# Kernel tuning notes

Measured on AMD Instinct MI355X. Metric: run time of the kernel, lower is better.

The kernel has to match this reference:

```python
import jax, jax.numpy as jnp
import numpy as np

N = 50000   # nodes
E = 800000  # edges
IN, HID, HEADS, OUT = 128, 32, 4, 64
NEG_SLOPE = 0.2


def _gatv2_layer(x, src, dst, Wl, bl, Wr, br, att, bias, res_W, concat):
    """One PyG-style GATv2Conv layer (eval mode, no dropout).
    x: [N, F_in]; att: [H, C]. Returns [N, H*C] if concat else [N, C]."""
    H, C = att.shape
    xl = (x @ Wl + bl).reshape(N, H, C)   # source transform
    xr = (x @ Wr + br).reshape(N, H, C)   # target transform
    e = jax.nn.leaky_relu(xl[src] + xr[dst], NEG_SLOPE)        # [E, H, C]
    logit = jnp.einsum('ehc,hc->eh', e, att)                   # [E, H]
    # segment softmax over incoming edges per destination node
    m = jax.ops.segment_max(logit, dst, num_segments=N)        # [N, H]
    p = jnp.exp(logit - m[dst])
    denom = jax.ops.segment_sum(p, dst, num_segments=N)
    alpha = p / (denom[dst] + 1e-16)                           # [E, H]
    out = jax.ops.segment_sum(xl[src] * alpha[:, :, None], dst, num_segments=N)  # [N, H, C]
    out = out.reshape(N, H * C) if concat else out.mean(axis=1)
    if res_W is not None:
        out = out + x @ res_W
    return out + bias


def _glorot(key, shape):
    fan_in = shape[0] if len(shape) > 1 else shape[-1]
    return jax.random.normal(key, shape, dtype=jnp.float32) / np.sqrt(fan_in)


def setup_inputs() -> dict:
    key = jax.random.key(0)
    ks = iter(jax.random.split(key, 32))
    x = jax.random.normal(next(ks), (N, IN), dtype=jnp.float32)
    edge_index = jax.random.randint(next(ks), (2, E), 0, N, dtype=jnp.int64)
    d = {"x": x, "edge_index": edge_index}
    HC = HEADS * HID  # 128
    # layer 0: IN -> HEADS*HID, concat, residual
    d["Wl0"] = _glorot(next(ks), (IN, HC)); d["bl0"] = jnp.zeros((HC,), jnp.float32)
    d["Wr0"] = _glorot(next(ks), (IN, HC)); d["br0"] = jnp.zeros((HC,), jnp.float32)
    d["att0"] = _glorot(next(ks), (HEADS, HID)); d["b0"] = jnp.zeros((HC,), jnp.float32)
    d["res0"] = _glorot(next(ks), (IN, HC))
    # layer 1: HC -> HEADS*HID, concat, residual
    d["Wl1"] = _glorot(next(ks), (HC, HC)); d["bl1"] = jnp.zeros((HC,), jnp.float32)
    d["Wr1"] = _glorot(next(ks), (HC, HC)); d["br1"] = jnp.zeros((HC,), jnp.float32)
    d["att1"] = _glorot(next(ks), (HEADS, HID)); d["b1"] = jnp.zeros((HC,), jnp.float32)
    d["res1"] = _glorot(next(ks), (HC, HC))
    # layer 2: HC -> OUT, heads=1, concat=False, no residual
    d["Wl2"] = _glorot(next(ks), (HC, OUT)); d["bl2"] = jnp.zeros((OUT,), jnp.float32)
    d["Wr2"] = _glorot(next(ks), (HC, OUT)); d["br2"] = jnp.zeros((OUT,), jnp.float32)
    d["att2"] = _glorot(next(ks), (1, OUT)); d["b2"] = jnp.zeros((OUT,), jnp.float32)
    return d


def reference(x, edge_index,
              Wl0, bl0, Wr0, br0, att0, b0, res0,
              Wl1, bl1, Wr1, br1, att1, b1, res1,
              Wl2, bl2, Wr2, br2, att2, b2):
    src, dst = edge_index[0], edge_index[1]
    h = _gatv2_layer(x, src, dst, Wl0, bl0, Wr0, br0, att0, b0, res0, True)
    h = jax.nn.elu(h)
    h = _gatv2_layer(h, src, dst, Wl1, bl1, Wr1, br1, att1, b1, res1, True)
    h = jax.nn.elu(h)
    return _gatv2_layer(h, src, dst, Wl2, bl2, Wr2, br2, att2, b2, None, False)
```

## Files before the change

### kernel.cpp

```cpp
#include <hip/hip_runtime.h>
#include <math.h>

#define NN 50000
#define EE 800000
#define NBK 196
#define EPB 4096

typedef short v8s __attribute__((ext_vector_type(8)));
typedef float v4f __attribute__((ext_vector_type(4)));

__device__ __forceinline__ ushort f2bf(float f) {
    uint u = __float_as_uint(f);
    uint r = (u + 0x7fffu + ((u >> 16) & 1u)) >> 16;
    return (ushort)r;
}
__device__ __forceinline__ float bf2f(ushort h) {
    return __uint_as_float(((uint)h) << 16);
}
__device__ __forceinline__ float lrelu(float x) {
    return fmaf(0.4f, fabsf(x), 0.6f * x);
}

__device__ __forceinline__ void gld_lds16(const void* g, void* l) {
    __builtin_amdgcn_global_load_lds(
        (const __attribute__((address_space(1))) void*)g,
        (__attribute__((address_space(3))) void*)l, 16, 0, 0);
}

template <int CTRL>
__device__ __forceinline__ float dppadd(float x) {
    int y = __builtin_amdgcn_update_dpp(0, __float_as_int(x), CTRL, 0xf, 0xf, true);
    return x + __int_as_float(y);
}
__device__ __forceinline__ float sum8(float x) {
    x = dppadd<0xB1>(x);
    x = dppadd<0x4E>(x);
    x = dppadd<0x141>(x);
    return x;
}
__device__ __forceinline__ float sum16(float x) {
    x = sum8(x);
    x = dppadd<0x140>(x);
    return x;
}
__device__ __forceinline__ float expclamp(float t) {
    return __expf(fminf(fmaxf(t, -60.f), 80.f));
}

__global__ __launch_bounds__(256) void k_bktcnt(const int* __restrict__ edst,
                                                int* __restrict__ bcnt) {
    __shared__ int h[NBK];
    int t = threadIdx.x;
    if (t < NBK) h[t] = 0;
    __syncthreads();
    int eb = blockIdx.x * EPB;
    #pragma unroll
    for (int k = 0; k < EPB / 256; ++k) {
        int e = eb + k * 256 + t;
        if (e < EE) atomicAdd(&h[edst[e] >> 8], 1);
    }
    __syncthreads();
    if (t < NBK && h[t]) atomicAdd(&bcnt[t], h[t]);
}

__global__ __launch_bounds__(256) void k_bscan(const int* __restrict__ bcnt,
                                               int* __restrict__ bbase,
                                               int* __restrict__ bcur) {
    __shared__ int sm[256];
    int t = threadIdx.x;
    int v = (t < NBK) ? bcnt[t] : 0;
    sm[t] = v;
    __syncthreads();
    for (int o = 1; o < 256; o <<= 1) {
        int a = (t >= o) ? sm[t - o] : 0;
        __syncthreads();
        sm[t] += a;
        __syncthreads();
    }
    if (t < NBK) { int ex = sm[t] - v; bbase[t] = ex; bcur[t] = ex; }
}

__global__ __launch_bounds__(256) void k_bktplace(const int* __restrict__ esrc,
                                                  const int* __restrict__ edst,
                                                  int* __restrict__ bcur,
                                                  uint* __restrict__ ebuf) {
    __shared__ int h[NBK];
    __shared__ int base[NBK];
    int t = threadIdx.x;
    if (t < NBK) h[t] = 0;
    __syncthreads();
    int eb = blockIdx.x * EPB;
    int pk[EPB / 256];
    #pragma unroll
    for (int k = 0; k < EPB / 256; ++k) {
        int e = eb + k * 256 + t;
        pk[k] = -1;
        if (e < EE) {
            int b = edst[e] >> 8;
            int r = atomicAdd(&h[b], 1);
            pk[k] = (b << 16) | r;
        }
    }
    __syncthreads();
    if (t < NBK && h[t]) base[t] = atomicAdd(&bcur[t], h[t]);
    __syncthreads();
    #pragma unroll
    for (int k = 0; k < EPB / 256; ++k) {
        int e = eb + k * 256 + t;
        if (e < EE) {
            int b = pk[k] >> 16;
            int r = pk[k] & 0xFFFF;
            uint dl = (uint)(edst[e] & 255);
            ebuf[base[b] + r] = (dl << 16) | (uint)esrc[e];
        }
    }
}

__global__ __launch_bounds__(256) void k_bktfin(const uint* __restrict__ ebuf,
                                                const int* __restrict__ bbase,
                                                const int* __restrict__ bcnt,
                                                int* __restrict__ rowptr,
                                                int* __restrict__ csrc) {
    __shared__ int deg[256];
    __shared__ int sm[256];
    __shared__ int cur[256];
    const int b = blockIdx.x;
    const int t = threadIdx.x;
    const int eb = bbase[b];
    const int ec = bcnt[b];
    deg[t] = 0;
    __syncthreads();
    for (int k = t; k < ec; k += 256)
        atomicAdd(&deg[ebuf[eb + k] >> 16], 1);
    __syncthreads();
    int v = deg[t];
    sm[t] = v;
    __syncthreads();
    for (int o = 1; o < 256; o <<= 1) {
        int a = (t >= o) ? sm[t - o] : 0;
        __syncthreads();
        sm[t] += a;
        __syncthreads();
    }
    int node = b * 256 + t;
    if (node < NN) rowptr[node + 1] = eb + sm[t];
    if (node == 0) rowptr[0] = 0;
    cur[t] = sm[t] - v;
    __syncthreads();
    for (int k = t; k < ec; k += 256) {
        uint u = ebuf[eb + k];
        int nl = (int)(u >> 16);
        int r = atomicAdd(&cur[nl], 1);
        csrc[eb + r] = (int)(u & 0xFFFFu);
    }
}

struct WPack {
    const float* W[8];
    ushort* Th[8];
    ushort* Tl[8];
    int fout[8];
};

__global__ __launch_bounds__(256) void k_conv_w(WPack p) {
    int wi = blockIdx.y;
    int fout = p.fout[wi];
    int total = 128 * fout;
    int i = blockIdx.x * 256 + threadIdx.x;
    if (i >= total) return;
    int k = i / fout;
    int n = i - k * fout;
    float f = p.W[wi][i];
    ushort h = f2bf(f);
    float lo = f - bf2f(h);
    int t = n >> 4, m = n & 15, c = k >> 5, quad = (k >> 3) & 3, j = k & 7;
    int flat = ((((t * 4 + c) * 4 + quad) * 16 + m) << 3) + j;
    p.Th[wi][flat] = h;
    p.Tl[wi][flat] = f2bf(lo);
}

template <int FOUT, int NMAT, bool CVT, int TS>
__global__ __launch_bounds__(512) void k_gemm_fused(
    const float* __restrict__ Xf,
    const ushort* __restrict__ Xh, const ushort* __restrict__ Xl,
    const ushort* __restrict__ T0h, const ushort* __restrict__ T0l, const float* __restrict__ B0,
    const ushort* __restrict__ T1h, const ushort* __restrict__ T1l, const float* __restrict__ B1,
    const ushort* __restrict__ T2h, const ushort* __restrict__ T2l,
    const float* __restrict__ ATT, float* __restrict__ DL, float* __restrict__ DR,
    ushort* __restrict__ O0b, float* __restrict__ O1, float* __restrict__ O2)
{
    constexpr int CH = TS * 2048;
    __shared__ __align__(16) ushort Bs[NMAT * 2 * CH];

    const int tid  = threadIdx.x;
    const int lane = tid & 63;
    const int wid  = tid >> 6;
    const int m    = lane & 15;
    const int quad = lane >> 4;
    const int row0 = blockIdx.x * 128 + wid * 16;
    const int t0   = blockIdx.y * TS;

    {
        const ushort* tbls[6] = {T0h, T0l, T1h, T1l, T2h, T2l};
        #pragma unroll
        for (int k = 0; k < 2 * NMAT; ++k) {
            gld_lds16(tbls[k] + (size_t)t0 * 2048 + (size_t)tid * 8,
                      &Bs[k * CH + tid * 8]);
        }
    }

    v8s ah[4], al[4];
    {
        int arow = row0 + m;
        if (arow > NN - 1) arow = NN - 1;
        #pragma unroll
        for (int c = 0; c < 4; ++c) {
            size_t off = (size_t)arow * 128 + c * 32 + quad * 8;
            if constexpr (CVT) {
                float4 f0 = *(const float4*)(Xf + off);
                float4 f1 = *(const float4*)(Xf + off + 4);
                const float fe[8] = {f0.x, f0.y, f0.z, f0.w, f1.x, f1.y, f1.z, f1.w};
                #pragma unroll
                for (int e = 0; e < 8; ++e) {
                    ushort h = f2bf(fe[e]);
                    float lo = fe[e] - bf2f(h);
                    ah[c][e] = (short)h;
                    al[c][e] = (short)(__float_as_uint(lo) >> 16);
                }
            } else {
                ah[c] = *(const v8s*)(Xh + off);
                al[c] = *(const v8s*)(Xl + off);
            }
        }
    }

    __syncthreads();

    float dp0[4] = {0.f, 0.f, 0.f, 0.f};
    float dp1[4] = {0.f, 0.f, 0.f, 0.f};

    #pragma unroll
    for (int tt = 0; tt < TS; ++tt) {
        const int t = t0 + tt;
        v4f a0 = {0.f, 0.f, 0.f, 0.f};
        v4f a1 = {0.f, 0.f, 0.f, 0.f};
        v4f a2 = {0.f, 0.f, 0.f, 0.f};
        #pragma unroll
        for (int c = 0; c < 4; ++c) {
            const int fo = tt * 2048 + (c * 4 + quad) * 128 + m * 8;
            v8s b0h = *(const v8s*)&Bs[0 * CH + fo];
            v8s b0l = *(const v8s*)&Bs[1 * CH + fo];
            v8s b1h = *(const v8s*)&Bs[2 * CH + fo];
            v8s b1l = *(const v8s*)&Bs[3 * CH + fo];
            a0 = __builtin_amdgcn_mfma_f32_16x16x32_bf16(al[c], b0h, a0, 0, 0, 0);
            a1 = __builtin_amdgcn_mfma_f32_16x16x32_bf16(al[c], b1h, a1, 0, 0, 0);
            a0 = __builtin_amdgcn_mfma_f32_16x16x32_bf16(ah[c], b0l, a0, 0, 0, 0);
            a1 = __builtin_amdgcn_mfma_f32_16x16x32_bf16(ah[c], b1l, a1, 0, 0, 0);
            a0 = __builtin_amdgcn_mfma_f32_16x16x32_bf16(ah[c], b0h, a0, 0, 0, 0);
            a1 = __builtin_amdgcn_mfma_f32_16x16x32_bf16(ah[c], b1h, a1, 0, 0, 0);
            if constexpr (NMAT == 3) {
                v8s b2h = *(const v8s*)&Bs[4 * CH + fo];
                v8s b2l = *(const v8s*)&Bs[5 * CH + fo];
                a2 = __builtin_amdgcn_mfma_f32_16x16x32_bf16(al[c], b2h, a2, 0, 0, 0);
                a2 = __builtin_amdgcn_mfma_f32_16x16x32_bf16(ah[c], b2l, a2, 0, 0, 0);
                a2 = __builtin_amdgcn_mfma_f32_16x16x32_bf16(ah[c], b2h, a2, 0, 0, 0);
            }
        }
        const int col = t * 16 + m;
        const float bad0 = B0[col];
        const float bad1 = B1[col];
        const float attc = ATT[col];
        #pragma unroll
        for (int j = 0; j < 4; ++j) {
            float o0v = a0[j] + bad0;
            float o1v = a1[j] + bad1;
            dp0[j] = fmaf(attc, o0v, dp0[j]);
            dp1[j] = fmaf(attc, o1v, dp1[j]);
            int r = row0 + quad * 4 + j;
            if (r < NN) {
                O0b[(size_t)r * FOUT + col] = f2bf(o0v);
                O1[(size_t)r * FOUT + col] = o1v;
                if constexpr (NMAT == 3) O2[(size_t)r * FOUT + col] = a2[j];
            }
        }
        if constexpr (FOUT == 128) {
            if ((t & 1) == 1) {
                const int h = t >> 1;
                #pragma unroll
                for (int j = 0; j < 4; ++j) {
                    float s0 = sum16(dp0[j]);
                    float s1 = sum16(dp1[j]);
                    int r = row0 + quad * 4 + j;
                    if (m == 0 && r < NN) {
                        DL[(size_t)r * 4 + h] = 0.6f * s0;
                        DR[(size_t)r * 4 + h] = 0.6f * s1;
                    }
                    dp0[j] = 0.f;
                    dp1[j] = 0.f;
                }
            }
        }
    }
    if constexpr (FOUT == 64) {
        #pragma unroll
        for (int j = 0; j < 4; ++j) {
            float s0 = sum16(dp0[j]);
            float s1 = sum16(dp1[j]);
            int r = row0 + quad * 4 + j;
            if (m == 0 && r < NN) {
                atomicAdd(&DL[r], 0.6f * s0);
                atomicAdd(&DR[r], 0.6f * s1);
            }
        }
    }
}

__global__ __launch_bounds__(256) void k_agg01(const ushort* __restrict__ XLb,
                                               const float4* __restrict__ XR4,
                                               const float4* __restrict__ RES4,
                                               const float* __restrict__ att,
                                               const float* __restrict__ bias,
                                               const float* __restrict__ DL,
                                               const float* __restrict__ DR,
                                               const int* __restrict__ rowptr,
                                               const int* __restrict__ csrc,
                                               ushort* __restrict__ Hh,
                                               ushort* __restrict__ Hl) {
    const int lane = threadIdx.x & 63;
    const int wid = threadIdx.x >> 6;
    const int n = blockIdx.x * 4 + wid;
    if (n >= NN) return;
    const int beg = rowptr[n];
    const int end = rowptr[n + 1];
    const int half = lane >> 5;
    const uint j = lane & 31;
    const uint head = j >> 3;

    const float4 xr = XR4[(uint)n * 32u + j];
    float4 at = ((const float4*)att)[j];
    at.x *= 0.4f; at.y *= 0.4f; at.z *= 0.4f; at.w *= 0.4f;
    const float dRn = DR[(uint)n * 4u + head];
    float4 s = {0.f, 0.f, 0.f, 0.f};
    float d = 0.f;

#define EDGE01(U, DLV)  {                                             \
    float4 v = {bf2f((U).x), bf2f((U).y), bf2f((U).z), bf2f((U).w)};  \
    float t0 =      at.x * fabsf(v.x + xr.x);                         \
    t0 = fmaf(at.y, fabsf(v.y + xr.y), t0);                           \
    t0 = fmaf(at.z, fabsf(v.z + xr.z), t0);                           \
    t0 = fmaf(at.w, fabsf(v.w + xr.w), t0);                           \
    float p = expclamp(sum8(t0) + (DLV) + dRn);                       \
    d += p;                                                            \
    s.x = fmaf(p, v.x, s.x); s.y = fmaf(p, v.y, s.y);                 \
    s.z = fmaf(p, v.z, s.z); s.w = fmaf(p, v.w, s.w); }

    int i = beg;
    for (; i + 8 <= end; i += 8) {
        uint sa = (uint)csrc[i + half];
        uint sb = (uint)csrc[i + 2 + half];
        uint sc = (uint)csrc[i + 4 + half];
        uint sd = (uint)csrc[i + 6 + half];
        ushort4 ua = *(const ushort4*)(XLb + (size_t)sa * 128u + 4u * j);
        float  da_ = DL[(size_t)sa * 4u + head];
        ushort4 ub = *(const ushort4*)(XLb + (size_t)sb * 128u + 4u * j);
        float  db_ = DL[(size_t)sb * 4u + head];
        ushort4 uc = *(const ushort4*)(XLb + (size_t)sc * 128u + 4u * j);
        float  dc_ = DL[(size_t)sc * 4u + head];
        ushort4 ud = *(const ushort4*)(XLb + (size_t)sd * 128u + 4u * j);
        float  dd_ = DL[(size_t)sd * 4u + head];
        EDGE01(ua, da_)
        EDGE01(ub, db_)
        EDGE01(uc, dc_)
        EDGE01(ud, dd_)
    }
    for (; i < end; i += 2) {
        int ia = i + half;
        if (ia > end - 1) ia = end - 1;
        uint sa = (uint)csrc[ia];
        ushort4 ua = *(const ushort4*)(XLb + (size_t)sa * 128u + 4u * j);
        float  da_ = DL[(size_t)sa * 4u + head];
        float4 v = {bf2f(ua.x), bf2f(ua.y), bf2f(ua.z), bf2f(ua.w)};
        float t0 =      at.x * fabsf(v.x + xr.x);
        t0 = fmaf(at.y, fabsf(v.y + xr.y), t0);
        t0 = fmaf(at.z, fabsf(v.z + xr.z), t0);
        t0 = fmaf(at.w, fabsf(v.w + xr.w), t0);
        float p = expclamp(sum8(t0) + da_ + dRn);
        if (half && (i + 1 >= end)) p = 0.f;
        d += p;
        s.x = fmaf(p, v.x, s.x); s.y = fmaf(p, v.y, s.y);
        s.z = fmaf(p, v.z, s.z); s.w = fmaf(p, v.w, s.w);
    }
#undef EDGE01

    d   += __shfl_xor(d, 32);
    s.x += __shfl_xor(s.x, 32);
    s.y += __shfl_xor(s.y, 32);
    s.z += __shfl_xor(s.z, 32);
    s.w += __shfl_xor(s.w, 32);

    if (half == 0) {
        float inv = (d > 0.f) ? 1.f / d : 0.f;
        float4 rv = RES4[(uint)n * 32u + j];
        float4 bv = ((const float4*)bias)[j];
        float o0 = fmaf(s.x, inv, rv.x + bv.x);
        float o1 = fmaf(s.y, inv, rv.y + bv.y);
        float o2 = fmaf(s.z, inv, rv.z + bv.z);
        float o3 = fmaf(s.w, inv, rv.w + bv.w);
        o0 = o0 > 0.f ? o0 : __expf(o0) - 1.f;
        o1 = o1 > 0.f ? o1 : __expf(o1) - 1.f;
        o2 = o2 > 0.f ? o2 : __expf(o2) - 1.f;
        o3 = o3 > 0.f ? o3 : __expf(o3) - 1.f;
        ushort4 h, l;
        h.x = f2bf(o0); l.x = f2bf(o0 - bf2f(h.x));
        h.y = f2bf(o1); l.y = f2bf(o1 - bf2f(h.y));
        h.z = f2bf(o2); l.z = f2bf(o2 - bf2f(h.z));
        h.w = f2bf(o3); l.w = f2bf(o3 - bf2f(h.w));
        *(ushort4*)(Hh + (uint)n * 128u + 4u * j) = h;
        *(ushort4*)(Hl + (uint)n * 128u + 4u * j) = l;
    }
}

__global__ __launch_bounds__(256) void k_agg2(const ushort* __restrict__ XLb,
                                              const float4* __restrict__ XR4,
                                              const float* __restrict__ att,
                                              const float* __restrict__ bias,
                                              const float* __restrict__ DL,
                                              const float* __restrict__ DR,
                                              const int* __restrict__ rowptr,
                                              const int* __restrict__ csrc,
                                              float* __restrict__ OUT) {
    const int lane = threadIdx.x & 63;
    const int wid = threadIdx.x >> 6;
    const int n = blockIdx.x * 4 + wid;
    if (n >= NN) return;
    const int beg = rowptr[n];
    const int end = rowptr[n + 1];
    const int q = lane >> 4;
    const uint jj = lane & 15;

    const float4 xr = XR4[(uint)n * 16u + jj];
    float4 at = ((const float4*)att)[jj];
    at.x *= 0.4f; at.y *= 0.4f; at.z *= 0.4f; at.w *= 0.4f;
    const float dRn = DR[n];
    float4 s = {0.f, 0.f, 0.f, 0.f};
    float d = 0.f;
    const int e1 = end - 1;

    for (int i = beg; i < end; i += 8) {
        int i0 = i + q;
        int i1 = i + 4 + q;
        uint s0 = (uint)csrc[min(i0, e1)];
        uint s1 = (uint)csrc[min(i1, e1)];
        ushort4 u0 = *(const ushort4*)(XLb + (size_t)s0 * 64u + 4u * jj);
        float  dl0 = DL[s0];
        ushort4 u1 = *(const ushort4*)(XLb + (size_t)s1 * 64u + 4u * jj);
        float  dl1 = DL[s1];
        #pragma unroll
        for (int u = 0; u < 2; ++u) {
            ushort4 uv = (u == 0) ? u0 : u1;
            float  dlv = (u == 0) ? dl0 : dl1;
            int ii = (u == 0) ? i0 : i1;
            float4 v = {bf2f(uv.x), bf2f(uv.y), bf2f(uv.z), bf2f(uv.w)};
            float t0 =      at.x * fabsf(v.x + xr.x);
            t0 = fmaf(at.y, fabsf(v.y + xr.y), t0);
            t0 = fmaf(at.z, fabsf(v.z + xr.z), t0);
            t0 = fmaf(at.w, fabsf(v.w + xr.w), t0);
            float p = expclamp(sum16(t0) + dlv + dRn);
            if (ii >= end) p = 0.f;
            d += p;
            s.x = fmaf(p, v.x, s.x); s.y = fmaf(p, v.y, s.y);
            s.z = fmaf(p, v.z, s.z); s.w = fmaf(p, v.w, s.w);
        }
    }

    d   += __shfl_xor(d, 16);   d   += __shfl_xor(d, 32);
    s.x += __shfl_xor(s.x, 16); s.x += __shfl_xor(s.x, 32);
    s.y += __shfl_xor(s.y, 16); s.y += __shfl_xor(s.y, 32);
    s.z += __shfl_xor(s.z, 16); s.z += __shfl_xor(s.z, 32);
    s.w += __shfl_xor(s.w, 16); s.w += __shfl_xor(s.w, 32);

    if (lane < 16) {
        float inv = (d > 0.f) ? 1.f / d : 0.f;
        float4 bv = ((const float4*)bias)[jj];
        float4 o;
        o.x = fmaf(s.x, inv, bv.x);
        o.y = fmaf(s.y, inv, bv.y);
        o.z = fmaf(s.z, inv, bv.z);
        o.w = fmaf(s.w, inv, bv.w);
        *(float4*)(OUT + (uint)n * 64u + 4u * jj) = o;
    }
}

extern "C" void kernel_launch(void* const* d_in, const int* in_sizes, int n_in,
                              void* d_out, int out_size, void* d_ws, size_t ws_size,
                              hipStream_t stream) {
    const float* x    = (const float*)d_in[0];
    const int*   ei   = (const int*)d_in[1];
    const int*   esrc = ei;
    const int*   edst = ei + EE;

    const float* Wl0 = (const float*)d_in[2];
    const float* bl0 = (const float*)d_in[3];
    const float* Wr0 = (const float*)d_in[4];
    const float* br0 = (const float*)d_in[5];
    const float* at0 = (const float*)d_in[6];
    const float* b0  = (const float*)d_in[7];
    const float* rs0 = (const float*)d_in[8];
    const float* Wl1 = (const float*)d_in[9];
    const float* bl1 = (const float*)d_in[10];
    const float* Wr1 = (const float*)d_in[11];
    const float* br1 = (const float*)d_in[12];
    const float* at1 = (const float*)d_in[13];
    const float* b1  = (const float*)d_in[14];
    const float* rs1 = (const float*)d_in[15];
    const float* Wl2 = (const float*)d_in[16];
    const float* bl2 = (const float*)d_in[17];
    const float* Wr2 = (const float*)d_in[18];
    const float* br2 = (const float*)d_in[19];
    const float* at2 = (const float*)d_in[20];
    const float* b2  = (const float*)d_in[21];

    float* out = (float*)d_out;

    ushort* XLb = (ushort*)d_ws;
    float* XR  = (float*)(XLb + (size_t)NN * 128);
    float* RES = XR + (size_t)NN * 128;
    ushort* Xh = (ushort*)(RES + (size_t)NN * 128);
    ushort* Xl_ = Xh + (size_t)NN * 128;
    float* DLarr = (float*)(Xl_ + (size_t)NN * 128);
    float* DRarr = DLarr + (size_t)NN * 4;
    ushort* Wth = (ushort*)(DRarr + (size_t)NN * 4);
    const int wsz[8] = {16384, 16384, 16384, 16384, 16384, 16384, 8192, 8192};
    ushort* th[8]; ushort* tl[8];
    {
        ushort* p = Wth;
        for (int i = 0; i < 8; ++i) { th[i] = p; p += wsz[i]; }
        for (int i = 0; i < 8; ++i) { tl[i] = p; p += wsz[i]; }
    }
    int* bcnt   = (int*)(Wth + 2 * (6 * 16384 + 2 * 8192));
    int* bbase  = bcnt + 256;
    int* bcur   = bbase + 256;
    int* rowptr = bcur + 256;
    int* csrc   = rowptr + (NN + 1);
    uint* ebuf  = (uint*)(csrc + EE);

    hipMemsetAsync(bcnt, 0, 256 * sizeof(int), stream);
    const int ebk = (EE + EPB - 1) / EPB;
    k_bktcnt<<<ebk, 256, 0, stream>>>(edst, bcnt);
    k_bscan<<<1, 256, 0, stream>>>(bcnt, bbase, bcur);
    k_bktplace<<<ebk, 256, 0, stream>>>(esrc, edst, bcur, ebuf);
    k_bktfin<<<NBK, 256, 0, stream>>>(ebuf, bbase, bcnt, rowptr, csrc);

    WPack wp;
    const float* Ws[8] = {Wl0, Wr0, rs0, Wl1, Wr1, rs1, Wl2, Wr2};
    const int fouts[8] = {128, 128, 128, 128, 128, 128, 64, 64};
    for (int i = 0; i < 8; ++i) { wp.W[i] = Ws[i]; wp.Th[i] = th[i]; wp.Tl[i] = tl[i]; wp.fout[i] = fouts[i]; }
    k_conv_w<<<dim3(64, 8), 256, 0, stream>>>(wp);

    const int gemm_gx = (NN + 127) / 128;
    const int agg_grid = (NN + 3) / 4;

    k_gemm_fused<128, 3, true, 2><<<dim3(gemm_gx, 4), 512, 0, stream>>>(x, nullptr, nullptr,
        th[0], tl[0], bl0, th[1], tl[1], br0, th[2], tl[2], at0, DLarr, DRarr, XLb, XR, RES);
    k_agg01<<<agg_grid, 256, 0, stream>>>(XLb, (const float4*)XR, (const float4*)RES,
        at0, b0, DLarr, DRarr, rowptr, csrc, Xh, Xl_);

    k_gemm_fused<128, 3, false, 2><<<dim3(gemm_gx, 4), 512, 0, stream>>>(nullptr, Xh, Xl_,
        th[3], tl[3], bl1, th[4], tl[4], br1, th[5], tl[5], at1, DLarr, DRarr, XLb, XR, RES);
    k_agg01<<<agg_grid, 256, 0, stream>>>(XLb, (const float4*)XR, (const float4*)RES,
        at1, b1, DLarr, DRarr, rowptr, csrc, Xh, Xl_);

    hipMemsetAsync(DLarr, 0, NN * sizeof(float), stream);
    hipMemsetAsync(DRarr, 0, NN * sizeof(float), stream);
    k_gemm_fused<64, 2, false, 2><<<dim3(gemm_gx, 2), 512, 0, stream>>>(nullptr, Xh, Xl_,
        th[6], tl[6], bl2, th[7], tl[7], br2, nullptr, nullptr, at2, DLarr, DRarr, XLb, XR, nullptr);
    k_agg2<<<agg_grid, 256, 0, stream>>>(XLb, (const float4*)XR, at2, b2, DLarr, DRarr, rowptr, csrc, out);
}
```

Baseline: 359.1 us.

## Widen per-lane feature chunks to 8 bf16 so each wave processes more edges in parallel

Both aggregation kernels now give each lane 8 bf16 features (16-byte loads) instead of 4, so one wave covers 4 edges at once in layers 0/1 and 8 in layer 2. This halves the lanes per edge row, which shortens the DPP reductions and issues fewer, wider gathers. The cost is more registers per lane, longer cross-group shuffle reductions at the end, and more wasted lanes on low-degree nodes. The main loop also loses its separate remainder path and masks out-of-range edges instead.

```diff
diff --git a/kernel.cpp b/kernel.cpp
--- a/kernel.cpp
+++ b/kernel.cpp
@@ -31,6 +31,11 @@
 __device__ __forceinline__ float dppadd(float x) {
     int y = __builtin_amdgcn_update_dpp(0, __float_as_int(x), CTRL, 0xf, 0xf, true);
     return x + __int_as_float(y);
+}
+__device__ __forceinline__ float sum4(float x) {
+    x = dppadd<0xB1>(x);
+    x = dppadd<0x4E>(x);
+    return x;
 }
 __device__ __forceinline__ float sum8(float x) {
     x = dppadd<0xB1>(x);
@@ -332,91 +337,98 @@
     if (n >= NN) return;
     const int beg = rowptr[n];
     const int end = rowptr[n + 1];
-    const int half = lane >> 5;
-    const uint j = lane & 31;
-    const uint head = j >> 3;
-
-    const float4 xr = XR4[(uint)n * 32u + j];
-    float4 at = ((const float4*)att)[j];
-    at.x *= 0.4f; at.y *= 0.4f; at.z *= 0.4f; at.w *= 0.4f;
+    const int q = lane >> 4;
+    const uint jj = lane & 15;
+    const uint head = jj >> 2;
+
+    const float4 xrA = XR4[(uint)n * 32u + 2u * jj];
+    const float4 xrB = XR4[(uint)n * 32u + 2u * jj + 1u];
+    float4 atA = ((const float4*)att)[2u * jj];
+    float4 atB = ((const float4*)att)[2u * jj + 1u];
+    atA.x *= 0.4f; atA.y *= 0.4f; atA.z *= 0.4f; atA.w *= 0.4f;
+    atB.x *= 0.4f; atB.y *= 0.4f; atB.z *= 0.4f; atB.w *= 0.4f;
     const float dRn = DR[(uint)n * 4u + head];
-    float4 s = {0.f, 0.f, 0.f, 0.f};
+    float s0_ = 0.f, s1_ = 0.f, s2_ = 0.f, s3_ = 0.f;
+    float s4_ = 0.f, s5_ = 0.f, s6_ = 0.f, s7_ = 0.f;
     float d = 0.f;
-
-#define EDGE01(U, DLV)  {                                             \
-    float4 v = {bf2f((U).x), bf2f((U).y), bf2f((U).z), bf2f((U).w)};  \
-    float t0 =      at.x * fabsf(v.x + xr.x);                         \
-    t0 = fmaf(at.y, fabsf(v.y + xr.y), t0);                           \
-    t0 = fmaf(at.z, fabsf(v.z + xr.z), t0);                           \
-    t0 = fmaf(at.w, fabsf(v.w + xr.w), t0);                           \
-    float p = expclamp(sum8(t0) + (DLV) + dRn);                       \
-    d += p;                                                            \
-    s.x = fmaf(p, v.x, s.x); s.y = fmaf(p, v.y, s.y);                 \
-    s.z = fmaf(p, v.z, s.z); s.w = fmaf(p, v.w, s.w); }
-
-    int i = beg;
-    for (; i + 8 <= end; i += 8) {
-        uint sa = (uint)csrc[i + half];
-        uint sb = (uint)csrc[i + 2 + half];
-        uint sc = (uint)csrc[i + 4 + half];
-        uint sd = (uint)csrc[i + 6 + half];
-        ushort4 ua = *(const ushort4*)(XLb + (size_t)sa * 128u + 4u * j);
-        float  da_ = DL[(size_t)sa * 4u + head];
-        ushort4 ub = *(const ushort4*)(XLb + (size_t)sb * 128u + 4u * j);
-        float  db_ = DL[(size_t)sb * 4u + head];
-        ushort4 uc = *(const ushort4*)(XLb + (size_t)sc * 128u + 4u * j);
-        float  dc_ = DL[(size_t)sc * 4u + head];
-        ushort4 ud = *(const ushort4*)(XLb + (size_t)sd * 128u + 4u * j);
-        float  dd_ = DL[(size_t)sd * 4u + head];
-        EDGE01(ua, da_)
-        EDGE01(ub, db_)
-        EDGE01(uc, dc_)
-        EDGE01(ud, dd_)
-    }
-    for (; i < end; i += 2) {
-        int ia = i + half;
-        if (ia > end - 1) ia = end - 1;
-        uint sa = (uint)csrc[ia];
-        ushort4 ua = *(const ushort4*)(XLb + (size_t)sa * 128u + 4u * j);
-        float  da_ = DL[(size_t)sa * 4u + head];
-        float4 v = {bf2f(ua.x), bf2f(ua.y), bf2f(ua.z), bf2f(ua.w)};
-        float t0 =      at.x * fabsf(v.x + xr.x);
-        t0 = fmaf(at.y, fabsf(v.y + xr.y), t0);
-        t0 = fmaf(at.z, fabsf(v.z + xr.z), t0);
-        t0 = fmaf(at.w, fabsf(v.w + xr.w), t0);
-        float p = expclamp(sum8(t0) + da_ + dRn);
-        if (half && (i + 1 >= end)) p = 0.f;
-        d += p;
-        s.x = fmaf(p, v.x, s.x); s.y = fmaf(p, v.y, s.y);
-        s.z = fmaf(p, v.z, s.z); s.w = fmaf(p, v.w, s.w);
-    }
-#undef EDGE01
-
-    d   += __shfl_xor(d, 32);
-    s.x += __shfl_xor(s.x, 32);
-    s.y += __shfl_xor(s.y, 32);
-    s.z += __shfl_xor(s.z, 32);
-    s.w += __shfl_xor(s.w, 32);
-
-    if (half == 0) {
+    const int e1 = end - 1;
+
+#define PROC01(U, DLV, II) {                                   \
+    float v0 = __uint_as_float((U).x << 16);                   \
+    float v1 = __uint_as_float((U).x & 0xFFFF0000u);           \
+    float v2 = __uint_as_float((U).y << 16);                   \
+    float v3 = __uint_as_float((U).y & 0xFFFF0000u);           \
+    float v4 = __uint_as_float((U).z << 16);                   \
+    float v5 = __uint_as_float((U).z & 0xFFFF0000u);           \
+    float v6 = __uint_as_float((U).w << 16);                   \
+    float v7 = __uint_as_float((U).w & 0xFFFF0000u);           \
+    float t =      atA.x * fabsf(v0 + xrA.x);                  \
+    t = fmaf(atA.y, fabsf(v1 + xrA.y), t);                     \
+    t = fmaf(atA.z, fabsf(v2 + xrA.z), t);                     \
+    t = fmaf(atA.w, fabsf(v3 + xrA.w), t);                     \
+    t = fmaf(atB.x, fabsf(v4 + xrB.x), t);                     \
+    t = fmaf(atB.y, fabsf(v5 + xrB.y), t);                     \
+    t = fmaf(atB.z, fabsf(v6 + xrB.z), t);                     \
+    t = fmaf(atB.w, fabsf(v7 + xrB.w), t);                     \
+    t = sum4(t);                                               \
+    float p = expclamp(t + (DLV) + dRn);                       \
+    if ((II) >= end) p = 0.f;                                  \
+    d += p;                                                    \
+    s0_ = fmaf(p, v0, s0_); s1_ = fmaf(p, v1, s1_);            \
+    s2_ = fmaf(p, v2, s2_); s3_ = fmaf(p, v3, s3_);            \
+    s4_ = fmaf(p, v4, s4_); s5_ = fmaf(p, v5, s5_);            \
+    s6_ = fmaf(p, v6, s6_); s7_ = fmaf(p, v7, s7_); }
+
+    for (int i = beg; i < end; i += 8) {
+        int i0 = i + q;
+        int i1 = i + 4 + q;
+        uint sa = (uint)csrc[min(i0, e1)];
+        uint sb = (uint)csrc[min(i1, e1)];
+        uint4 Ua = *(const uint4*)(XLb + sa * 128u + 8u * jj);
+        float da_ = DL[sa * 4u + head];
+        uint4 Ub = *(const uint4*)(XLb + sb * 128u + 8u * jj);
+        float db_ = DL[sb * 4u + head];
+        PROC01(Ua, da_, i0)
+        PROC01(Ub, db_, i1)
+    }
+#undef PROC01
+
+    d   += __shfl_xor(d, 16);   d   += __shfl_xor(d, 32);
+    s0_ += __shfl_xor(s0_, 16); s0_ += __shfl_xor(s0_, 32);
+    s1_ += __shfl_xor(s1_, 16); s1_ += __shfl_xor(s1_, 32);
+    s2_ += __shfl_xor(s2_, 16); s2_ += __shfl_xor(s2_, 32);
+    s3_ += __shfl_xor(s3_, 16); s3_ += __shfl_xor(s3_, 32);
+    s4_ += __shfl_xor(s4_, 16); s4_ += __shfl_xor(s4_, 32);
+    s5_ += __shfl_xor(s5_, 16); s5_ += __shfl_xor(s5_, 32);
+    s6_ += __shfl_xor(s6_, 16); s6_ += __shfl_xor(s6_, 32);
+    s7_ += __shfl_xor(s7_, 16); s7_ += __shfl_xor(s7_, 32);
+
+    if (q == 0) {
         float inv = (d > 0.f) ? 1.f / d : 0.f;
-        float4 rv = RES4[(uint)n * 32u + j];
-        float4 bv = ((const float4*)bias)[j];
-        float o0 = fmaf(s.x, inv, rv.x + bv.x);
-        float o1 = fmaf(s.y, inv, rv.y + bv.y);
-        float o2 = fmaf(s.z, inv, rv.z + bv.z);
-        float o3 = fmaf(s.w, inv, rv.w + bv.w);
-        o0 = o0 > 0.f ? o0 : __expf(o0) - 1.f;
-        o1 = o1 > 0.f ? o1 : __expf(o1) - 1.f;
-        o2 = o2 > 0.f ? o2 : __expf(o2) - 1.f;
-        o3 = o3 > 0.f ? o3 : __expf(o3) - 1.f;
-        ushort4 h, l;
-        h.x = f2bf(o0); l.x = f2bf(o0 - bf2f(h.x));
-        h.y = f2bf(o1); l.y = f2bf(o1 - bf2f(h.y));
-        h.z = f2bf(o2); l.z = f2bf(o2 - bf2f(h.z));
-        h.w = f2bf(o3); l.w = f2bf(o3 - bf2f(h.w));
-        *(ushort4*)(Hh + (uint)n * 128u + 4u * j) = h;
-        *(ushort4*)(Hl + (uint)n * 128u + 4u * j) = l;
+        const float4 rA = RES4[(uint)n * 32u + 2u * jj];
+        const float4 rB = RES4[(uint)n * 32u + 2u * jj + 1u];
+        const float4 bA = ((const float4*)bias)[2u * jj];
+        const float4 bB = ((const float4*)bias)[2u * jj + 1u];
+        float o[8];
+        o[0] = fmaf(s0_, inv, rA.x + bA.x);
+        o[1] = fmaf(s1_, inv, rA.y + bA.y);
+        o[2] = fmaf(s2_, inv, rA.z + bA.z);
+        o[3] = fmaf(s3_, inv, rA.w + bA.w);
+        o[4] = fmaf(s4_, inv, rB.x + bB.x);
+        o[5] = fmaf(s5_, inv, rB.y + bB.y);
+        o[6] = fmaf(s6_, inv, rB.z + bB.z);
+        o[7] = fmaf(s7_, inv, rB.w + bB.w);
+        v8s hh, ll;
+        #pragma unroll
+        for (int c = 0; c < 8; ++c) {
+            float ov = o[c];
+            ov = ov > 0.f ? ov : __expf(ov) - 1.f;
+            ushort h = f2bf(ov);
+            hh[c] = (short)h;
+            ll[c] = (short)f2bf(ov - bf2f(h));
+        }
+        *(v8s*)(Hh + (uint)n * 128u + 8u * jj) = hh;
+        *(v8s*)(Hl + (uint)n * 128u + 8u * jj) = ll;
     }
 }
 
@@ -435,59 +447,86 @@
     if (n >= NN) return;
     const int beg = rowptr[n];
     const int end = rowptr[n + 1];
-    const int q = lane >> 4;
-    const uint jj = lane & 15;
-
-    const float4 xr = XR4[(uint)n * 16u + jj];
-    float4 at = ((const float4*)att)[jj];
-    at.x *= 0.4f; at.y *= 0.4f; at.z *= 0.4f; at.w *= 0.4f;
+    const int q = lane >> 3;
+    const uint jj = lane & 7;
+
+    const float4 xrA = XR4[(uint)n * 16u + 2u * jj];
+    const float4 xrB = XR4[(uint)n * 16u + 2u * jj + 1u];
+    float4 atA = ((const float4*)att)[2u * jj];
+    float4 atB = ((const float4*)att)[2u * jj + 1u];
+    atA.x *= 0.4f; atA.y *= 0.4f; atA.z *= 0.4f; atA.w *= 0.4f;
+    atB.x *= 0.4f; atB.y *= 0.4f; atB.z *= 0.4f; atB.w *= 0.4f;
     const float dRn = DR[n];
-    float4 s = {0.f, 0.f, 0.f, 0.f};
+    float s0_ = 0.f, s1_ = 0.f, s2_ = 0.f, s3_ = 0.f;
+    float s4_ = 0.f, s5_ = 0.f, s6_ = 0.f, s7_ = 0.f;
     float d = 0.f;
     const int e1 = end - 1;
 
-    for (int i = beg; i < end; i += 8) {
+#define PROC2(U, DLV, II) {                                    \
+    float v0 = __uint_as_float((U).x << 16);                   \
+    float v1 = __uint_as_float((U).x & 0xFFFF0000u);           \
+    float v2 = __uint_as_float((U).y << 16);                   \
+    float v3 = __uint_as_float((U).y & 0xFFFF0000u);           \
+    float v4 = __uint_as_float((U).z << 16);                   \
+    float v5 = __uint_as_float((U).z & 0xFFFF0000u);           \
+    float v6 = __uint_as_float((U).w << 16);                   \
+    float v7 = __uint_as_float((U).w & 0xFFFF0000u);           \
+    float t =      atA.x * fabsf(v0 + xrA.x);                  \
+    t = fmaf(atA.y, fabsf(v1 + xrA.y), t);                     \
+    t = fmaf(atA.z, fabsf(v2 + xrA.z), t);                     \
+    t = fmaf(atA.w, fabsf(v3 + xrA.w), t);                     \
+    t = fmaf(atB.x, fabsf(v4 + xrB.x), t);                     \
+    t = fmaf(atB.y, fabsf(v5 + xrB.y), t);                     \
+    t = fmaf(atB.z, fabsf(v6 + xrB.z), t);                     \
+    t = fmaf(atB.w, fabsf(v7 + xrB.w), t);                     \
+    t = sum8(t);                                               \
+    float p = expclamp(t + (DLV) + dRn);                       \
+    if ((II) >= end) p = 0.f;                                  \
+    d += p;                                                    \
+    s0_ = fmaf(p, v0, s0_); s1_ = fmaf(p, v1, s1_);            \
+    s2_ = fmaf(p, v2, s2_); s3_ = fmaf(p, v3, s3_);            \
+    s4_ = fmaf(p, v4, s4_); s5_ = fmaf(p, v5, s5_);            \
+    s6_ = fmaf(p, v6, s6_); s7_ = fmaf(p, v7, s7_); }
+
+    for (int i = beg; i < end; i += 16) {
         int i0 = i + q;
-        int i1 = i + 4 + q;
-        uint s0 = (uint)csrc[min(i0, e1)];
-        uint s1 = (uint)csrc[min(i1, e1)];
-        ushort4 u0 = *(const ushort4*)(XLb + (size_t)s0 * 64u + 4u * jj);
-        float  dl0 = DL[s0];
-        ushort4 u1 = *(const ushort4*)(XLb + (size_t)s1 * 64u + 4u * jj);
-        float  dl1 = DL[s1];
-        #pragma unroll
-        for (int u = 0; u < 2; ++u) {
-            ushort4 uv = (u == 0) ? u0 : u1;
-            float  dlv = (u == 0) ? dl0 : dl1;
-            int ii = (u == 0) ? i0 : i1;
-            float4 v = {bf2f(uv.x), bf2f(uv.y), bf2f(uv.z), bf2f(uv.w)};
-            float t0 =      at.x * fabsf(v.x + xr.x);
-            t0 = fmaf(at.y, fabsf(v.y + xr.y), t0);
-            t0 = fmaf(at.z, fabsf(v.z + xr.z), t0);
-            t0 = fmaf(at.w, fabsf(v.w + xr.w), t0);
-            float p = expclamp(sum16(t0) + dlv + dRn);
-            if (ii >= end) p = 0.f;
-            d += p;
-            s.x = fmaf(p, v.x, s.x); s.y = fmaf(p, v.y, s.y);
-            s.z = fmaf(p, v.z, s.z); s.w = fmaf(p, v.w, s.w);
-        }
-    }
-
-    d   += __shfl_xor(d, 16);   d   += __shfl_xor(d, 32);
-    s.x += __shfl_xor(s.x, 16); s.x += __shfl_xor(s.x, 32);
-    s.y += __shfl_xor(s.y, 16); s.y += __shfl_xor(s.y, 32);
-    s.z += __shfl_xor(s.z, 16); s.z += __shfl_xor(s.z, 32);
-    s.w += __shfl_xor(s.w, 16); s.w += __shfl_xor(s.w, 32);
-
-    if (lane < 16) {
+        int i1 = i + 8 + q;
+        uint sa = (uint)csrc[min(i0, e1)];
+        uint sb = (uint)csrc[min(i1, e1)];
+        uint4 Ua = *(const uint4*)(XLb + sa * 64u + 8u * jj);
+        float da_ = DL[sa];
+        uint4 Ub = *(const uint4*)(XLb + sb * 64u + 8u * jj);
+        float db_ = DL[sb];
+        PROC2(Ua, da_, i0)
+        PROC2(Ub, db_, i1)
+    }
+#undef PROC2
+
+    d   += __shfl_xor(d, 8);    d   += __shfl_xor(d, 16);   d   += __shfl_xor(d, 32);
+    s0_ += __shfl_xor(s0_, 8);  s0_ += __shfl_xor(s0_, 16); s0_ += __shfl_xor(s0_, 32);
+    s1_ += __shfl_xor(s1_, 8);  s1_ += __shfl_xor(s1_, 16); s1_ += __shfl_xor(s1_, 32);
+    s2_ += __shfl_xor(s2_, 8);  s2_ += __shfl_xor(s2_, 16); s2_ += __shfl_xor(s2_, 32);
+    s3_ += __shfl_xor(s3_, 8);  s3_ += __shfl_xor(s3_, 16); s3_ += __shfl_xor(s3_, 32);
+    s4_ += __shfl_xor(s4_, 8);  s4_ += __shfl_xor(s4_, 16); s4_ += __shfl_xor(s4_, 32);
+    s5_ += __shfl_xor(s5_, 8);  s5_ += __shfl_xor(s5_, 16); s5_ += __shfl_xor(s5_, 32);
+    s6_ += __shfl_xor(s6_, 8);  s6_ += __shfl_xor(s6_, 16); s6_ += __shfl_xor(s6_, 32);
+    s7_ += __shfl_xor(s7_, 8);  s7_ += __shfl_xor(s7_, 16); s7_ += __shfl_xor(s7_, 32);
+
+    if (lane < 8) {
         float inv = (d > 0.f) ? 1.f / d : 0.f;
-        float4 bv = ((const float4*)bias)[jj];
-        float4 o;
-        o.x = fmaf(s.x, inv, bv.x);
-        o.y = fmaf(s.y, inv, bv.y);
-        o.z = fmaf(s.z, inv, bv.z);
-        o.w = fmaf(s.w, inv, bv.w);
-        *(float4*)(OUT + (uint)n * 64u + 4u * jj) = o;
+        const float4 bA = ((const float4*)bias)[2u * jj];
+        const float4 bB = ((const float4*)bias)[2u * jj + 1u];
+        float4 oA, oB;
+        oA.x = fmaf(s0_, inv, bA.x);
+        oA.y = fmaf(s1_, inv, bA.y);
+        oA.z = fmaf(s2_, inv, bA.z);
+        oA.w = fmaf(s3_, inv, bA.w);
+        oB.x = fmaf(s4_, inv, bB.x);
+        oB.y = fmaf(s5_, inv, bB.y);
+        oB.z = fmaf(s6_, inv, bB.z);
+        oB.w = fmaf(s7_, inv, bB.w);
+        *(float4*)(OUT + (uint)n * 64u + 8u * jj) = oA;
+        *(float4*)(OUT + (uint)n * 64u + 8u * jj + 4u) = oB;
     }
 }
 
```

New measurement: 371.0 us. +3.3%, slower.
